# Performance work log

Measured on AMD Instinct MI355X. Metric: run time of the kernel, lower is better.

Reference implementation:

```python
import jax, jax.numpy as jnp
import numpy as np

MP = 0.0   # positive-pair margin (init kwarg mp)
MN = 1.0   # negative-pair margin (init kwarg mn)
EPS = 1e-07


def setup_inputs() -> dict:
    key = jax.random.key(0)
    k1, k2 = jax.random.split(key)
    n, d = 8192, 128
    embeddings = jax.random.normal(k1, (n, d), dtype=jnp.float32)
    labels = jax.random.randint(k2, (n,), 0, 100, dtype=jnp.int64)
    return {"embeddings": embeddings, "labels": labels}


def reference(embeddings, labels):
    n = embeddings.shape[0]
    # Pairwise L2 distances via Gram matrix (same math as norm(x[:,None]-x),
    # without the O(n^2 d) broadcast intermediate).
    sq = jnp.sum(embeddings * embeddings, axis=1)              # [n]
    gram = embeddings @ embeddings.T                           # [n, n]
    d2 = sq[:, None] + sq[None, :] - 2.0 * gram                # [n, n]
    mask = jnp.triu(jnp.ones((n, n), dtype=bool), k=1)         # strict upper tri
    d2_safe = jnp.where(mask, jnp.maximum(d2, 0.0), 1.0)       # guard sqrt grad
    dist = jnp.sqrt(d2_safe)                                   # L2 distance
    # Original applies sqrt AGAIN to the distance (quirk of the source): keep it.
    dists = jnp.sqrt(dist + EPS)
    same = labels[:, None] == labels[None, :]
    loss = jnp.where(same,
                     jnp.maximum(dists - MP, 0.0),
                     jnp.maximum(MN - dists, 0.0))
    num_pairs = n * (n - 1) // 2
    return jnp.sum(jnp.where(mask, loss, 0.0)) / num_pairs
```

## Files before the change

kernel.cpp:

```cpp
#include <hip/hip_runtime.h>
#include <hip/hip_bf16.h>
#include <stdint.h>

typedef __attribute__((ext_vector_type(8))) short short8;
typedef __attribute__((ext_vector_type(4))) float f32x4;

__device__ __forceinline__ unsigned int f2bf(float f) {
    unsigned int u = __float_as_uint(f);
    return (u + 0x7fffu + ((u >> 16) & 1u)) >> 16;
}

__global__ void prep_kernel(const float* __restrict__ emb,
                            unsigned short* __restrict__ ebs,
                            float* __restrict__ sq, int n) {
    int t = threadIdx.x;
    int row = blockIdx.x * 16 + (t >> 4);
    int c   = t & 15;
    if (row >= n) return;
    const float* src = emb + (size_t)row * 128 + c * 8;
    float4 f0 = *reinterpret_cast<const float4*>(src);
    float4 f1 = *reinterpret_cast<const float4*>(src + 4);
    uint4 wv;
    wv.x = f2bf(f0.x) | (f2bf(f0.y) << 16);
    wv.y = f2bf(f0.z) | (f2bf(f0.w) << 16);
    wv.z = f2bf(f1.x) | (f2bf(f1.y) << 16);
    wv.w = f2bf(f1.z) | (f2bf(f1.w) << 16);
    size_t byte = (size_t)(row >> 4) * 4096 + c * 256 + (row & 15) * 16;
    *reinterpret_cast<uint4*>(reinterpret_cast<char*>(ebs) + byte) = wv;
    float p = f0.x*f0.x + f0.y*f0.y + f0.z*f0.z + f0.w*f0.w
            + f1.x*f1.x + f1.y*f1.y + f1.z*f1.z + f1.w*f1.w;
    #pragma unroll
    for (int off = 1; off < 16; off <<= 1) p += __shfl_xor(p, off);
    if (c == 0) sq[row] = p;
}

__launch_bounds__(256, 4)
__global__ void loss_kernel(const unsigned short* __restrict__ ebs,
                            const int* __restrict__ labels,
                            const float* __restrict__ sq,
                            float* __restrict__ partials) {
    __shared__ float wsum[4];

    int id = blockIdx.x;
    int bj = (int)((sqrtf(8.0f * (float)id + 1.0f) - 1.0f) * 0.5f);
    while (((bj + 1) * (bj + 2)) >> 1 <= id) ++bj;
    while (((bj * (bj + 1)) >> 1) > id) --bj;
    int bi = id - ((bj * (bj + 1)) >> 1);
    int rowBase = bi << 6, colBase = bj << 6;
    bool offdiag = (bi != bj);

    int t = threadIdx.x, lane = t & 63, w = t >> 6;
    int wr = (w & 1) << 5, wc = (w >> 1) << 5;
    int fr = lane & 15, kg = lane >> 4, lo = lane << 4;

    const char* base = reinterpret_cast<const char*>(ebs);
    const char* gA = base + (size_t)((rowBase + wr) >> 4) * 4096;
    const char* gB = base + (size_t)((colBase + wc) >> 4) * 4096;

    short8 a[2][4], b[2][4];
    #pragma unroll
    for (int kk = 0; kk < 4; ++kk) {
        a[0][kk] = *reinterpret_cast<const short8*>(gA        + kk * 1024 + lo);
        a[1][kk] = *reinterpret_cast<const short8*>(gA + 4096 + kk * 1024 + lo);
        b[0][kk] = *reinterpret_cast<const short8*>(gB        + kk * 1024 + lo);
        b[1][kk] = *reinterpret_cast<const short8*>(gB + 4096 + kk * 1024 + lo);
    }

    float4 sqi[2]; int4 labi[2];
    #pragma unroll
    for (int m = 0; m < 2; ++m) {
        int irb = rowBase + wr + m * 16 + kg * 4;
        sqi[m]  = *reinterpret_cast<const float4*>(sq + irb);
        labi[m] = *reinterpret_cast<const int4*>(labels + irb);
    }
    float sqj0  = sq[colBase + wc + fr];
    float sqj1  = sq[colBase + wc + 16 + fr];
    int   labj0 = labels[colBase + wc + fr];
    int   labj1 = labels[colBase + wc + 16 + fr];

    f32x4 acc[2][2];
    const f32x4 zero = {0.0f, 0.0f, 0.0f, 0.0f};
    acc[0][0] = zero; acc[0][1] = zero; acc[1][0] = zero; acc[1][1] = zero;

    #pragma unroll
    for (int kk = 0; kk < 4; ++kk) {
        acc[0][0] = __builtin_amdgcn_mfma_f32_16x16x32_bf16(a[0][kk], b[0][kk], acc[0][0], 0, 0, 0);
        acc[0][1] = __builtin_amdgcn_mfma_f32_16x16x32_bf16(a[0][kk], b[1][kk], acc[0][1], 0, 0, 0);
        acc[1][0] = __builtin_amdgcn_mfma_f32_16x16x32_bf16(a[1][kk], b[0][kk], acc[1][0], 0, 0, 0);
        acc[1][1] = __builtin_amdgcn_mfma_f32_16x16x32_bf16(a[1][kk], b[1][kk], acc[1][1], 0, 0, 0);
    }

    float l0 = 0.0f, l1 = 0.0f, l2 = 0.0f, l3 = 0.0f;

    #define EPI(PRED)                                                          \
    {                                                                          \
        _Pragma("unroll")                                                      \
        for (int m = 0; m < 2; ++m) {                                          \
            int irb = wr + m * 16 + kg * 4;                                    \
            _Pragma("unroll")                                                  \
            for (int nn = 0; nn < 2; ++nn) {                                   \
                float sj = nn ? sqj1 : sqj0;                                   \
                int   lj = nn ? labj1 : labj0;                                 \
                int   jc = wc + nn * 16 + fr; (void)jc;                        \
                _Pragma("unroll")                                              \
                for (int r4 = 0; r4 < 4; ++r4) {                               \
                    int ir = irb + r4; (void)ir;                               \
                    if (PRED) {                                                \
                        float si = (r4 == 0) ? sqi[m].x : (r4 == 1) ? sqi[m].y \
                                 : (r4 == 2) ? sqi[m].z : sqi[m].w;            \
                        int   li = (r4 == 0) ? labi[m].x : (r4 == 1) ? labi[m].y \
                                 : (r4 == 2) ? labi[m].z : labi[m].w;          \
                        float d2   = fmaf(-2.0f, acc[m][nn][r4], si + sj);     \
                        float dist = __builtin_amdgcn_sqrtf(fmaxf(d2, 0.0f));  \
                        float ds   = __builtin_amdgcn_sqrtf(dist + 1e-7f);     \
                        float v    = (li == lj) ? ds : fmaxf(1.0f - ds, 0.0f); \
                        if      (r4 == 0) l0 += v;                             \
                        else if (r4 == 1) l1 += v;                             \
                        else if (r4 == 2) l2 += v;                             \
                        else              l3 += v;                             \
                    }                                                          \
                }                                                              \
            }                                                                  \
        }                                                                      \
    }
    if (offdiag) EPI(true)
    else         EPI(jc > ir)
    #undef EPI

    float local = (l0 + l1) + (l2 + l3);
    #pragma unroll
    for (int off = 32; off > 0; off >>= 1) local += __shfl_down(local, off);
    if (lane == 0) wsum[w] = local;
    __syncthreads();
    if (t == 0)
        partials[blockIdx.x] = (wsum[0] + wsum[1]) + (wsum[2] + wsum[3]);
}

__launch_bounds__(1024)
__global__ void reduce_kernel(const float* __restrict__ partials, int nBlocks,
                              float* __restrict__ out, float inv_pairs) {
    __shared__ float ws[16];
    int t = threadIdx.x, lane = t & 63, w = t >> 6;
    float s = 0.0f;
    for (int i = t; i < nBlocks; i += 1024) s += partials[i];
    #pragma unroll
    for (int off = 32; off > 0; off >>= 1) s += __shfl_down(s, off);
    if (lane == 0) ws[w] = s;
    __syncthreads();
    if (w == 0) {
        float v = (lane < 16) ? ws[lane] : 0.0f;
        #pragma unroll
        for (int off = 8; off > 0; off >>= 1) v += __shfl_down(v, off);
        if (lane == 0) out[0] = v * inv_pairs;
    }
}

extern "C" void kernel_launch(void* const* d_in, const int* in_sizes, int n_in,
                              void* d_out, int out_size, void* d_ws, size_t ws_size,
                              hipStream_t stream) {
    const float* emb   = (const float*)d_in[0];
    const int*  labels = (const int*)d_in[1];
    int n  = in_sizes[1];
    int nt = n >> 6;

    float*          sq       = (float*)((char*)d_ws + 256);
    unsigned short* ebs      = (unsigned short*)((char*)d_ws + 65536);
    size_t          ebsBytes = (size_t)n * 128 * 2;
    float*          partials = (float*)((char*)d_ws + 65536 + ebsBytes);

    prep_kernel<<<n / 16, 256, 0, stream>>>(emb, ebs, sq, n);

    int nBlocks = nt * (nt + 1) / 2;
    loss_kernel<<<nBlocks, 256, 0, stream>>>(ebs, labels, sq, partials);

    float inv_pairs = (float)(2.0 / ((double)n * (double)(n - 1)));
    reduce_kernel<<<1, 1024, 0, stream>>>(partials, nBlocks, (float*)d_out, inv_pairs);
}
```

Before: 35.98 us.

## Enlarge triangular tiles to 128x128 with LDS-staged B and early-out sqrt skipping

Each block now handles a 128x128 tile instead of 64x64. The B columns are staged into LDS through global_load_lds and reused by all four waves, and each wave computes a 32-row strip across four 32-column sub-tiles. Diagonal blocks skip sub-tiles that lie fully below the diagonal. The epilogue skips the two sqrts when no lane in the wave needs them (a different-label pair with d2 >= 1 contributes zero), which adds a wave vote in exchange for less transcendental work. Bigger tiles mean fewer blocks and less redundant global traffic, but use 32KB of LDS per block and may reduce occupancy.

```diff
diff --git a/kernel.cpp b/kernel.cpp
--- a/kernel.cpp
+++ b/kernel.cpp
@@ -39,6 +39,7 @@
                             const int* __restrict__ labels,
                             const float* __restrict__ sq,
                             float* __restrict__ partials) {
+    __shared__ __align__(16) char Bs[32768];
     __shared__ float wsum[4];
 
     int id = blockIdx.x;
@@ -46,25 +47,34 @@
     while (((bj + 1) * (bj + 2)) >> 1 <= id) ++bj;
     while (((bj * (bj + 1)) >> 1) > id) --bj;
     int bi = id - ((bj * (bj + 1)) >> 1);
-    int rowBase = bi << 6, colBase = bj << 6;
+    int rowBase = bi << 7, colBase = bj << 7;
     bool offdiag = (bi != bj);
 
     int t = threadIdx.x, lane = t & 63, w = t >> 6;
-    int wr = (w & 1) << 5, wc = (w >> 1) << 5;
+    int wr = w << 5;
     int fr = lane & 15, kg = lane >> 4, lo = lane << 4;
 
     const char* base = reinterpret_cast<const char*>(ebs);
+
+    {
+        const char* gB = base + (size_t)(colBase >> 4) * 4096;
+        int thrOff = t << 4;
+        #pragma unroll
+        for (int it = 0; it < 8; ++it) {
+            int off = (it << 12) + thrOff;
+            __builtin_amdgcn_global_load_lds(
+                (const __attribute__((address_space(1))) void*)(gB + off),
+                (__attribute__((address_space(3))) void*)(Bs + off), 16, 0, 0);
+        }
+    }
+
     const char* gA = base + (size_t)((rowBase + wr) >> 4) * 4096;
-    const char* gB = base + (size_t)((colBase + wc) >> 4) * 4096;
-
-    short8 a[2][4], b[2][4];
-    #pragma unroll
-    for (int kk = 0; kk < 4; ++kk) {
-        a[0][kk] = *reinterpret_cast<const short8*>(gA        + kk * 1024 + lo);
-        a[1][kk] = *reinterpret_cast<const short8*>(gA + 4096 + kk * 1024 + lo);
-        b[0][kk] = *reinterpret_cast<const short8*>(gB        + kk * 1024 + lo);
-        b[1][kk] = *reinterpret_cast<const short8*>(gB + 4096 + kk * 1024 + lo);
-    }
+    short8 a[2][4];
+    #pragma unroll
+    for (int m = 0; m < 2; ++m)
+        #pragma unroll
+        for (int kk = 0; kk < 4; ++kk)
+            a[m][kk] = *reinterpret_cast<const short8*>(gA + m * 4096 + kk * 1024 + lo);
 
     float4 sqi[2]; int4 labi[2];
     #pragma unroll
@@ -73,59 +83,81 @@
         sqi[m]  = *reinterpret_cast<const float4*>(sq + irb);
         labi[m] = *reinterpret_cast<const int4*>(labels + irb);
     }
-    float sqj0  = sq[colBase + wc + fr];
-    float sqj1  = sq[colBase + wc + 16 + fr];
-    int   labj0 = labels[colBase + wc + fr];
-    int   labj1 = labels[colBase + wc + 16 + fr];
-
-    f32x4 acc[2][2];
-    const f32x4 zero = {0.0f, 0.0f, 0.0f, 0.0f};
-    acc[0][0] = zero; acc[0][1] = zero; acc[1][0] = zero; acc[1][1] = zero;
-
-    #pragma unroll
-    for (int kk = 0; kk < 4; ++kk) {
-        acc[0][0] = __builtin_amdgcn_mfma_f32_16x16x32_bf16(a[0][kk], b[0][kk], acc[0][0], 0, 0, 0);
-        acc[0][1] = __builtin_amdgcn_mfma_f32_16x16x32_bf16(a[0][kk], b[1][kk], acc[0][1], 0, 0, 0);
-        acc[1][0] = __builtin_amdgcn_mfma_f32_16x16x32_bf16(a[1][kk], b[0][kk], acc[1][0], 0, 0, 0);
-        acc[1][1] = __builtin_amdgcn_mfma_f32_16x16x32_bf16(a[1][kk], b[1][kk], acc[1][1], 0, 0, 0);
-    }
+
+    __syncthreads();
 
     float l0 = 0.0f, l1 = 0.0f, l2 = 0.0f, l3 = 0.0f;
 
-    #define EPI(PRED)                                                          \
-    {                                                                          \
-        _Pragma("unroll")                                                      \
-        for (int m = 0; m < 2; ++m) {                                          \
-            int irb = wr + m * 16 + kg * 4;                                    \
+    #pragma unroll
+    for (int s = 0; s < 4; ++s) {
+        int cs = s << 5;
+        if (!offdiag && cs + 32 <= wr) continue;
+
+        short8 b[2][4];
+        #pragma unroll
+        for (int nn = 0; nn < 2; ++nn)
+            #pragma unroll
+            for (int kk = 0; kk < 4; ++kk)
+                b[nn][kk] = *reinterpret_cast<const short8*>(
+                    Bs + ((cs >> 4) + nn) * 4096 + kk * 1024 + lo);
+
+        f32x4 acc[2][2];
+        const f32x4 zero = {0.0f, 0.0f, 0.0f, 0.0f};
+        acc[0][0] = zero; acc[0][1] = zero; acc[1][0] = zero; acc[1][1] = zero;
+        #pragma unroll
+        for (int kk = 0; kk < 4; ++kk) {
+            acc[0][0] = __builtin_amdgcn_mfma_f32_16x16x32_bf16(a[0][kk], b[0][kk], acc[0][0], 0, 0, 0);
+            acc[0][1] = __builtin_amdgcn_mfma_f32_16x16x32_bf16(a[0][kk], b[1][kk], acc[0][1], 0, 0, 0);
+            acc[1][0] = __builtin_amdgcn_mfma_f32_16x16x32_bf16(a[1][kk], b[0][kk], acc[1][0], 0, 0, 0);
+            acc[1][1] = __builtin_amdgcn_mfma_f32_16x16x32_bf16(a[1][kk], b[1][kk], acc[1][1], 0, 0, 0);
+        }
+
+        float sqj0  = sq[colBase + cs + fr];
+        float sqj1  = sq[colBase + cs + 16 + fr];
+        int   labj0 = labels[colBase + cs + fr];
+        int   labj1 = labels[colBase + cs + 16 + fr];
+
+        bool fullTile = offdiag || (cs >= wr + 32);
+
+        #define EPI(PREDEXPR)                                                  \
+        {                                                                      \
             _Pragma("unroll")                                                  \
-            for (int nn = 0; nn < 2; ++nn) {                                   \
-                float sj = nn ? sqj1 : sqj0;                                   \
-                int   lj = nn ? labj1 : labj0;                                 \
-                int   jc = wc + nn * 16 + fr; (void)jc;                        \
+            for (int m = 0; m < 2; ++m) {                                      \
+                int irb = wr + m * 16 + kg * 4;                                \
                 _Pragma("unroll")                                              \
-                for (int r4 = 0; r4 < 4; ++r4) {                               \
-                    int ir = irb + r4; (void)ir;                               \
-                    if (PRED) {                                                \
+                for (int nn = 0; nn < 2; ++nn) {                               \
+                    float sj = nn ? sqj1 : sqj0;                               \
+                    int   lj = nn ? labj1 : labj0;                             \
+                    int   jc = cs + nn * 16 + fr; (void)jc;                    \
+                    _Pragma("unroll")                                          \
+                    for (int r4 = 0; r4 < 4; ++r4) {                           \
+                        int ir = irb + r4; (void)ir;                           \
+                        bool pred = (PREDEXPR);                                \
                         float si = (r4 == 0) ? sqi[m].x : (r4 == 1) ? sqi[m].y \
                                  : (r4 == 2) ? sqi[m].z : sqi[m].w;            \
                         int   li = (r4 == 0) ? labi[m].x : (r4 == 1) ? labi[m].y \
                                  : (r4 == 2) ? labi[m].z : labi[m].w;          \
                         float d2   = fmaf(-2.0f, acc[m][nn][r4], si + sj);     \
-                        float dist = __builtin_amdgcn_sqrtf(fmaxf(d2, 0.0f));  \
-                        float ds   = __builtin_amdgcn_sqrtf(dist + 1e-7f);     \
-                        float v    = (li == lj) ? ds : fmaxf(1.0f - ds, 0.0f); \
-                        if      (r4 == 0) l0 += v;                             \
-                        else if (r4 == 1) l1 += v;                             \
-                        else if (r4 == 2) l2 += v;                             \
-                        else              l3 += v;                             \
+                        bool  same = (li == lj);                               \
+                        bool  need = pred && (same || (d2 < 1.0f));            \
+                        if (__any(need)) {                                     \
+                            float dist = __builtin_amdgcn_sqrtf(fmaxf(d2, 0.0f)); \
+                            float ds   = __builtin_amdgcn_sqrtf(dist + 1e-7f); \
+                            float v    = same ? ds : fmaxf(1.0f - ds, 0.0f);   \
+                            v = pred ? v : 0.0f;                               \
+                            if      (r4 == 0) l0 += v;                         \
+                            else if (r4 == 1) l1 += v;                         \
+                            else if (r4 == 2) l2 += v;                         \
+                            else              l3 += v;                         \
+                        }                                                      \
                     }                                                          \
                 }                                                              \
             }                                                                  \
-        }                                                                      \
-    }
-    if (offdiag) EPI(true)
-    else         EPI(jc > ir)
-    #undef EPI
+        }
+        if (fullTile) EPI(true)
+        else          EPI(jc > ir)
+        #undef EPI
+    }
 
     float local = (l0 + l1) + (l2 + l3);
     #pragma unroll
@@ -161,7 +193,7 @@
     const float* emb   = (const float*)d_in[0];
     const int*  labels = (const int*)d_in[1];
     int n  = in_sizes[1];
-    int nt = n >> 6;
+    int nt = n >> 7;
 
     float*          sq       = (float*)((char*)d_ws + 256);
     unsigned short* ebs      = (unsigned short*)((char*)d_ws + 65536);
```

Result: faster. 30.45 us (-15.4%).
